# Performance work log

Measured on AMD Instinct MI355X. Metric: run time of the kernel, lower is better.

Reference implementation:

```python
import jax, jax.numpy as jnp
import numpy as np

N, E = 50000, 800000
HID, EDGE_DIM, HEADS = 128, 16, 4
C = HID // HEADS  # 32
NEG_SLOPE = 0.2  # GATv2Conv default negative_slope


def setup_inputs() -> dict:
    key = jax.random.key(0)
    ks = jax.random.split(key, 16)
    def glorot(k, shape):
        fan_in = shape[0]
        return jax.random.normal(k, shape, jnp.float32) / np.sqrt(fan_in)
    return {
        "x": jax.random.normal(ks[0], (N, HID), jnp.float32),
        "edge_index": jax.random.randint(ks[1], (2, E), 0, N, jnp.int64 if jax.config.jax_enable_x64 else jnp.int32),
        "edge_attr": jax.random.normal(ks[2], (E, EDGE_DIM), jnp.float32),
        # GATv2Conv params (lin_l, lin_r with bias; lin_edge bias-free; att; final bias)
        "Wl": glorot(ks[3], (HID, HID)),
        "bl": jnp.zeros((HID,), jnp.float32),
        "Wr": glorot(ks[4], (HID, HID)),
        "br": jnp.zeros((HID,), jnp.float32),
        "We": glorot(ks[5], (EDGE_DIM, HID)),
        "att": glorot(ks[6], (HEADS, C)),
        "bias_gat": jnp.zeros((HID,), jnp.float32),
        # RMSNorm weights
        "w_norm1": jnp.ones((HID,), jnp.float32),
        "w_norm2": jnp.ones((HID,), jnp.float32),
        # FFN params
        "ffn_w1": glorot(ks[7], (HID, 4 * HID)),
        "ffn_b1": jnp.zeros((4 * HID,), jnp.float32),
        "ffn_w2": glorot(ks[8], (4 * HID, HID)),
        "ffn_b2": jnp.zeros((HID,), jnp.float32),
    }


def rmsnorm(x, w):
    # torch.nn.RMSNorm with eps=None -> eps = finfo(dtype).eps
    eps = jnp.finfo(x.dtype).eps
    ms = jnp.mean(x * x, axis=-1, keepdims=True)
    return x * jax.lax.rsqrt(ms + eps) * w


def gatv2_conv(x, edge_index, edge_attr, Wl, bl, Wr, br, We, att, bias_gat):
    n = x.shape[0]
    h, c = att.shape
    xl = (x @ Wl + bl).reshape(n, h, c)   # source-side transform (x_j)
    xr = (x @ Wr + br).reshape(n, h, c)   # target-side transform (x_i)
    src, dst = edge_index[0], edge_index[1]
    e = (edge_attr @ We).reshape(-1, h, c)
    m = xl[src] + xr[dst] + e                       # [E, H, C] per-edge message pre-activation
    s = jnp.where(m > 0, m, NEG_SLOPE * m)          # LeakyReLU(0.2)
    logits = jnp.einsum('ehc,hc->eh', s, att)       # [E, H]
    # scatter-softmax over edges grouped by target node
    lmax = jax.ops.segment_max(logits, dst, num_segments=n)
    ex = jnp.exp(logits - lmax[dst])
    den = jax.ops.segment_sum(ex, dst, num_segments=n)
    alpha = ex / (den[dst] + 1e-16)                 # PyG softmax denominator guard
    out = jax.ops.segment_sum(alpha[..., None] * xl[src], dst, num_segments=n)
    return out.reshape(n, h * c) + bias_gat


def reference(x, edge_index, edge_attr, Wl, bl, Wr, br, We, att, bias_gat,
              w_norm1, w_norm2, ffn_w1, ffn_b1, ffn_w2, ffn_b2):
    x_attn = gatv2_conv(x, edge_index, edge_attr, Wl, bl, Wr, br, We, att, bias_gat)
    h = rmsnorm(x + x_attn, w_norm1)
    f = jax.nn.gelu(h @ ffn_w1 + ffn_b1, approximate=False) @ ffn_w2 + ffn_b2
    return rmsnorm(h + f, w_norm2)
```

## Files before the change

kernel.cpp:

```cpp
#include <hip/hip_runtime.h>

#define NN 50000
#define EE 800000

typedef unsigned short u16;

#define OFF_GAT  0u
#define OFF_XLB  6400000u
#define OFF_XRB  9600000u
#define OFF_SRC  12800000u
#define OFF_EID  13600000u
#define OFF_CNT  14400000u
#define OFF_OFS  14450000u
#define OFF_H    6400000u
#define OFF_WLRT 14500004u
#define OFF_W1T  14516388u
#define OFF_W2T  14549156u

#define RMS_EPS 1.1920928955078125e-7f

typedef float f32x4v __attribute__((ext_vector_type(4)));
typedef short s16x8 __attribute__((ext_vector_type(8)));

__device__ __forceinline__ f32x4v mfma16(s16x8 a, s16x8 b, f32x4v c) {
  return __builtin_amdgcn_mfma_f32_16x16x32_bf16(a, b, c, 0, 0, 0);
}
__device__ __forceinline__ u16 f2b(float f) {
  unsigned int u = __float_as_uint(f);
  unsigned int r = (u + 0x7fffu + ((u >> 16) & 1u)) >> 16;
  return (u16)r;
}
__device__ __forceinline__ float b2f(u16 u) {
  union { float f; unsigned int i; } x; x.i = ((unsigned int)u) << 16; return x.f;
}
__device__ __forceinline__ s16x8 ld_bf16x8_f32(const float* __restrict__ p) {
  float4 v0 = *(const float4*)p;
  float4 v1 = *(const float4*)(p + 4);
  s16x8 r;
  r[0] = (short)f2b(v0.x); r[1] = (short)f2b(v0.y);
  r[2] = (short)f2b(v0.z); r[3] = (short)f2b(v0.w);
  r[4] = (short)f2b(v1.x); r[5] = (short)f2b(v1.y);
  r[6] = (short)f2b(v1.z); r[7] = (short)f2b(v1.w);
  return r;
}
__device__ __forceinline__ float readlane_f32(float v, int lane) {
  return __int_as_float(__builtin_amdgcn_readlane(__float_as_int(v), lane));
}
__device__ __forceinline__ int readlane_i32(int v, int lane) {
  return __builtin_amdgcn_readlane(v, lane);
}

__global__ __launch_bounds__(256) void k_zero(int* __restrict__ p, int n) {
  int i = blockIdx.x * 256 + threadIdx.x;
  if (i < n) p[i] = 0;
}
__global__ __launch_bounds__(256) void k_tcvt2(const float* __restrict__ Wl, const float* __restrict__ Wr,
                                               u16* __restrict__ out) {
  int i = blockIdx.x * 256 + threadIdx.x;
  int n = i >> 7, k = i & 127;
  float v = (n < 128) ? Wl[k * 128 + n] : Wr[k * 128 + (n - 128)];
  out[i] = f2b(v);
}
__global__ __launch_bounds__(256) void k_t1(const float* __restrict__ W1, u16* __restrict__ out) {
  int i = blockIdx.x * 256 + threadIdx.x;
  int n = i >> 7, k = i & 127;
  out[i] = f2b(W1[k * 512 + n]);
}
__global__ __launch_bounds__(256) void k_t2(const float* __restrict__ W2, u16* __restrict__ out) {
  int i = blockIdx.x * 256 + threadIdx.x;
  int n = i >> 9, k = i & 511;
  out[i] = f2b(W2[k * 128 + n]);
}

__global__ __launch_bounds__(256) void k_hist(const int* __restrict__ ei, int* __restrict__ cnt) {
  int e = blockIdx.x * 256 + threadIdx.x;
  if (e < EE) atomicAdd(&cnt[ei[EE + e]], 1);
}

__global__ __launch_bounds__(1024) void k_scan(const int* __restrict__ cnt,
    int* __restrict__ offs, int* __restrict__ pos)
{
  __shared__ int wsum[16];
  __shared__ int carry_s;
  int tid = threadIdx.x, lane = tid & 63, wv = tid >> 6;
  if (tid == 0) carry_s = 0;
  __syncthreads();
  for (int base = 0; base < NN; base += 1024) {
    int i = base + tid;
    int v = (i < NN) ? cnt[i] : 0;
    int x = v;
#pragma unroll
    for (int ofs = 1; ofs < 64; ofs <<= 1) {
      int y = __shfl_up(x, ofs);
      if (lane >= ofs) x += y;
    }
    if (lane == 63) wsum[wv] = x;
    __syncthreads();
    if (wv == 0) {
      int s = (lane < 16) ? wsum[lane] : 0;
#pragma unroll
      for (int ofs = 1; ofs < 16; ofs <<= 1) {
        int y = __shfl_up(s, ofs);
        if (lane >= ofs) s += y;
      }
      if (lane < 16) wsum[lane] = s;
    }
    __syncthreads();
    int wbase = (wv > 0) ? wsum[wv - 1] : 0;
    int incl = x + wbase + carry_s;
    if (i < NN) { offs[i + 1] = incl; pos[i] = incl - v; }
    if (base == 0 && tid == 0) offs[0] = 0;
    __syncthreads();
    if (tid == 1023) carry_s = incl;
    __syncthreads();
  }
}

__global__ __launch_bounds__(256) void k_permute(const int* __restrict__ ei,
    int* __restrict__ pos, int* __restrict__ srcarr, int* __restrict__ eidarr)
{
  int e = blockIdx.x * 256 + threadIdx.x;
  if (e < EE) {
    int slot = atomicAdd(&pos[ei[EE + e]], 1);
    srcarr[slot] = ei[e];
    eidarr[slot] = e;
  }
}

__global__ __launch_bounds__(256) void k1_mfma(const float* __restrict__ x, const u16* __restrict__ wlrt,
    const float* __restrict__ bl, const float* __restrict__ br,
    u16* __restrict__ xlb, u16* __restrict__ xrb)
{
  int tid = threadIdx.x;
  int w = tid >> 6, lane = tid & 63;
  int quad = lane >> 4, l16 = lane & 15;
  int row0 = blockIdx.x * 32;
  int ko = quad * 8;
  f32x4v acc[2][4];
#pragma unroll
  for (int mt = 0; mt < 2; ++mt)
#pragma unroll
    for (int nt = 0; nt < 4; ++nt) acc[mt][nt] = (f32x4v){0.f, 0.f, 0.f, 0.f};
#pragma unroll
  for (int ks = 0; ks < 4; ++ks) {
    int k0 = ks * 32 + ko;
    s16x8 a[2];
#pragma unroll
    for (int mt = 0; mt < 2; ++mt) {
      int row = row0 + mt * 16 + l16; if (row >= NN) row = NN - 1;
      a[mt] = ld_bf16x8_f32(x + row * 128 + k0);
    }
#pragma unroll
    for (int nt = 0; nt < 4; ++nt) {
      int col = w * 64 + nt * 16 + l16;
      s16x8 b = *(const s16x8*)(wlrt + col * 128 + k0);
      acc[0][nt] = mfma16(a[0], b, acc[0][nt]);
      acc[1][nt] = mfma16(a[1], b, acc[1][nt]);
    }
  }
#pragma unroll
  for (int nt = 0; nt < 4; ++nt) {
    int col = w * 64 + nt * 16 + l16;
    bool isl = col < 128;
    float bias = isl ? bl[col] : br[col - 128];
    u16* dst = isl ? xlb : xrb;
    int cc = isl ? col : col - 128;
#pragma unroll
    for (int mt = 0; mt < 2; ++mt)
#pragma unroll
      for (int r = 0; r < 4; ++r) {
        int row = row0 + mt * 16 + quad * 4 + r;
        if (row < NN) dst[row * 128 + cc] = f2b(acc[mt][nt][r] + bias);
      }
  }
}

__global__ __launch_bounds__(256) void k2_attn(
    const int* __restrict__ offs, const int* __restrict__ srcarr,
    const int* __restrict__ eidarr, const float* __restrict__ eattr,
    const float* __restrict__ att, const float* __restrict__ We,
    const u16* __restrict__ xlb, const u16* __restrict__ xrb,
    float* __restrict__ gat)
{
  int l = threadIdx.x & 63;
  int wid = (blockIdx.x * blockDim.x + threadIdx.x) >> 6;
  int nw = (gridDim.x * blockDim.x) >> 6;
  int c0 = 2 * l;
  const float2* We2 = (const float2*)We;
  float2 wef[16];
#pragma unroll
  for (int k = 0; k < 16; ++k) wef[k] = We2[k * 64 + l];
  float a0 = att[c0], a1 = att[c0 + 1];
  for (int d = wid; d < NN; d += nw) {
    int start = offs[d];
    int deg = offs[d + 1] - start;
    ushort2 xru = *(const ushort2*)(xrb + d * 128 + c0);
    float xr0 = b2f(xru.x), xr1 = b2f(xru.y);
    float mh = -1e30f, lh = 0.f, O0 = 0.f, O1 = 0.f;
    for (int base = 0; base < deg; base += 64) {
      bool act = (base + l) < deg;
      int idx = start + base + l;
      int sv = act ? srcarr[idx] : 0;
      int ev = act ? eidarr[idx] : 0;
      int cnt = min(64, deg - base);
      for (int sub = 0; sub < cnt; sub += 4) {
        int eidq = __shfl(ev, sub + (l >> 4));
        float eav = eattr[eidq * 16 + (l & 15)];
#pragma unroll
        for (int j2 = 0; j2 < 4; ++j2) {
          int j = sub + j2;
          if (j >= cnt) break;
          int sr = readlane_i32(sv, j);
          float ep0 = 0.f, ep1 = 0.f;
#pragma unroll
          for (int k = 0; k < 16; ++k) {
            float ek = readlane_f32(eav, j2 * 16 + k);
            ep0 = fmaf(ek, wef[k].x, ep0);
            ep1 = fmaf(ek, wef[k].y, ep1);
          }
          ushort2 xlu = *(const ushort2*)(xlb + sr * 128 + c0);
          float xl0 = b2f(xlu.x), xl1 = b2f(xlu.y);
          float m0 = xl0 + xr0 + ep0;
          float m1 = xl1 + xr1 + ep1;
          float s0 = m0 > 0.f ? m0 : 0.2f * m0;
          float s1 = m1 > 0.f ? m1 : 0.2f * m1;
          float p = fmaf(s0, a0, s1 * a1);
          p += __shfl_xor(p, 1); p += __shfl_xor(p, 2);
          p += __shfl_xor(p, 4); p += __shfl_xor(p, 8);
          float nm = fmaxf(mh, p);
          float sc = __expf(mh - nm);
          float wgt = __expf(p - nm);
          lh = lh * sc + wgt;
          O0 = fmaf(wgt, xl0, O0 * sc);
          O1 = fmaf(wgt, xl1, O1 * sc);
          mh = nm;
        }
      }
    }
    float inv = 1.f / (lh + 1e-16f);
    *(float2*)(gat + d * 128 + c0) = make_float2(O0 * inv, O1 * inv);
  }
}

__global__ __launch_bounds__(256) void k5_norm1(const float* __restrict__ x,
    const float* __restrict__ gat, const float* __restrict__ bg,
    const float* __restrict__ wn1, float* __restrict__ h)
{
  int l = threadIdx.x & 63;
  int row = blockIdx.x * 4 + (threadIdx.x >> 6);
  int c0 = 2 * l;
  float2 xu = *(const float2*)(x + row * 128 + c0);
  float2 gv = *(const float2*)(gat + row * 128 + c0);
  float2 bu = *(const float2*)(bg + c0);
  float v0 = xu.x + gv.x + bu.x;
  float v1 = xu.y + gv.y + bu.y;
  float ss = v0 * v0 + v1 * v1;
#pragma unroll
  for (int o = 1; o < 64; o <<= 1) ss += __shfl_xor(ss, o);
  float rr = rsqrtf(ss * (1.f / 128.f) + RMS_EPS);
  float2 wu = *(const float2*)(wn1 + c0);
  *(float2*)(h + row * 128 + c0) = make_float2(v0 * rr * wu.x, v1 * rr * wu.y);
}

__global__ __launch_bounds__(256) void k6_mfma(const float* __restrict__ h,
    const u16* __restrict__ w1t, const u16* __restrict__ w2t,
    const float* __restrict__ b1, const float* __restrict__ b2,
    const float* __restrict__ wn2, float* __restrict__ out)
{
  __shared__ u16 tls[32 * 520];
  __shared__ float red[4][32];
  int tid = threadIdx.x;
  int w = tid >> 6, lane = tid & 63;
  int quad = lane >> 4, l16 = lane & 15;
  int row0 = blockIdx.x * 32;
  int ko = quad * 8;

  f32x4v acc1[2][8];
#pragma unroll
  for (int mt = 0; mt < 2; ++mt)
#pragma unroll
    for (int nt = 0; nt < 8; ++nt) acc1[mt][nt] = (f32x4v){0.f, 0.f, 0.f, 0.f};
#pragma unroll
  for (int ks = 0; ks < 4; ++ks) {
    int k0 = ks * 32 + ko;
    s16x8 a[2];
#pragma unroll
    for (int mt = 0; mt < 2; ++mt) {
      int row = row0 + mt * 16 + l16; if (row >= NN) row = NN - 1;
      a[mt] = ld_bf16x8_f32(h + row * 128 + k0);
    }
#pragma unroll
    for (int nt = 0; nt < 8; ++nt) {
      int col = w * 128 + nt * 16 + l16;
      s16x8 b = *(const s16x8*)(w1t + col * 128 + k0);
      acc1[0][nt] = mfma16(a[0], b, acc1[0][nt]);
      acc1[1][nt] = mfma16(a[1], b, acc1[1][nt]);
    }
  }
#pragma unroll
  for (int nt = 0; nt < 8; ++nt) {
    int col = w * 128 + nt * 16 + l16;
    float bb = b1[col];
#pragma unroll
    for (int mt = 0; mt < 2; ++mt)
#pragma unroll
      for (int r = 0; r < 4; ++r) {
        float t = acc1[mt][nt][r] + bb;
        t = 0.5f * t * (1.f + erff(t * 0.70710678118654752f));
        tls[(mt * 16 + quad * 4 + r) * 520 + col] = f2b(t);
      }
  }
  __syncthreads();

  f32x4v acc2[2][2];
#pragma unroll
  for (int mt = 0; mt < 2; ++mt)
#pragma unroll
    for (int nt = 0; nt < 2; ++nt) acc2[mt][nt] = (f32x4v){0.f, 0.f, 0.f, 0.f};
#pragma unroll
  for (int ks = 0; ks < 16; ++ks) {
    int k0 = ks * 32 + ko;
    s16x8 a2[2];
#pragma unroll
    for (int mt = 0; mt < 2; ++mt)
      a2[mt] = *(const s16x8*)(tls + (mt * 16 + l16) * 520 + k0);
#pragma unroll
    for (int nt = 0; nt < 2; ++nt) {
      int col = w * 32 + nt * 16 + l16;
      s16x8 b = *(const s16x8*)(w2t + col * 512 + k0);
      acc2[0][nt] = mfma16(a2[0], b, acc2[0][nt]);
      acc2[1][nt] = mfma16(a2[1], b, acc2[1][nt]);
    }
  }
  int cols[2]; float bb2[2], wn[2];
#pragma unroll
  for (int nt = 0; nt < 2; ++nt) {
    cols[nt] = w * 32 + nt * 16 + l16;
    bb2[nt] = b2[cols[nt]];
    wn[nt] = wn2[cols[nt]];
  }
  float ov[2][2][4];
#pragma unroll
  for (int mt = 0; mt < 2; ++mt)
#pragma unroll
    for (int r = 0; r < 4; ++r) {
      int row = row0 + mt * 16 + quad * 4 + r;
      int rowc = row < NN ? row : NN - 1;
#pragma unroll
      for (int nt = 0; nt < 2; ++nt)
        ov[mt][nt][r] = h[rowc * 128 + cols[nt]] + acc2[mt][nt][r] + bb2[nt];
    }
#pragma unroll
  for (int mt = 0; mt < 2; ++mt)
#pragma unroll
    for (int r = 0; r < 4; ++r) {
      float q = ov[mt][0][r] * ov[mt][0][r] + ov[mt][1][r] * ov[mt][1][r];
      q += __shfl_xor(q, 1); q += __shfl_xor(q, 2);
      q += __shfl_xor(q, 4); q += __shfl_xor(q, 8);
      if (l16 == 0) red[w][mt * 16 + quad * 4 + r] = q;
    }
  __syncthreads();
#pragma unroll
  for (int mt = 0; mt < 2; ++mt)
#pragma unroll
    for (int r = 0; r < 4; ++r) {
      int rl = mt * 16 + quad * 4 + r;
      float tot = red[0][rl] + red[1][rl] + red[2][rl] + red[3][rl];
      float rr = rsqrtf(tot * (1.f / 128.f) + RMS_EPS);
      int row = row0 + rl;
      if (row < NN) {
        out[row * 128 + cols[0]] = ov[mt][0][r] * rr * wn[0];
        out[row * 128 + cols[1]] = ov[mt][1][r] * rr * wn[1];
      }
    }
}

extern "C" void kernel_launch(void* const* d_in, const int* in_sizes, int n_in,
                              void* d_out, int out_size, void* d_ws, size_t ws_size,
                              hipStream_t stream) {
  const float* x   = (const float*)d_in[0];
  const int*   ei  = (const int*)d_in[1];
  const float* ea  = (const float*)d_in[2];
  const float* Wl  = (const float*)d_in[3];
  const float* bl  = (const float*)d_in[4];
  const float* Wr  = (const float*)d_in[5];
  const float* br  = (const float*)d_in[6];
  const float* We  = (const float*)d_in[7];
  const float* att = (const float*)d_in[8];
  const float* bg  = (const float*)d_in[9];
  const float* wn1 = (const float*)d_in[10];
  const float* wn2 = (const float*)d_in[11];
  const float* W1  = (const float*)d_in[12];
  const float* b1  = (const float*)d_in[13];
  const float* W2  = (const float*)d_in[14];
  const float* b2  = (const float*)d_in[15];

  float* wsf = (float*)d_ws;
  int*   wsi = (int*)d_ws;

  float* gat  = wsf + OFF_GAT;
  u16* xlb    = (u16*)(wsf + OFF_XLB);
  u16* xrb    = (u16*)(wsf + OFF_XRB);
  int* srcarr = wsi + OFF_SRC;
  int* eidarr = wsi + OFF_EID;
  int* cnt    = wsi + OFF_CNT;
  int* pos    = wsi + OFF_CNT;
  int* offs   = wsi + OFF_OFS;
  float* hbuf = wsf + OFF_H;
  u16* wlrt   = (u16*)(wsf + OFF_WLRT);
  u16* w1t    = (u16*)(wsf + OFF_W1T);
  u16* w2t    = (u16*)(wsf + OFF_W2T);

  k_zero<<<(NN + 255) / 256, 256, 0, stream>>>(cnt, NN);
  k_tcvt2<<<128, 256, 0, stream>>>(Wl, Wr, wlrt);
  k_t1<<<256, 256, 0, stream>>>(W1, w1t);
  k_t2<<<256, 256, 0, stream>>>(W2, w2t);

  k_hist<<<(EE + 255) / 256, 256, 0, stream>>>(ei, cnt);
  k_scan<<<1, 1024, 0, stream>>>(cnt, offs, pos);
  k_permute<<<(EE + 255) / 256, 256, 0, stream>>>(ei, pos, srcarr, eidarr);

  k1_mfma<<<(NN + 31) / 32, 256, 0, stream>>>(x, wlrt, bl, br, xlb, xrb);

  k2_attn<<<1024, 256, 0, stream>>>(offs, srcarr, eidarr, ea, att, We, xlb, xrb, gat);

  k5_norm1<<<NN / 4, 256, 0, stream>>>(x, gat, bg, wn1, hbuf);

  k6_mfma<<<(NN + 31) / 32, 256, 0, stream>>>(hbuf, w1t, w2t, b1, b2, wn2, (float*)d_out);
}
```

Before: 586.9 us.

## Batch online-softmax updates per four edges, pack src/eid, fuse prep kernels

```diff
diff --git a/kernel.cpp b/kernel.cpp
--- a/kernel.cpp
+++ b/kernel.cpp
@@ -8,8 +8,7 @@
 #define OFF_GAT  0u
 #define OFF_XLB  6400000u
 #define OFF_XRB  9600000u
-#define OFF_SRC  12800000u
-#define OFF_EID  13600000u
+#define OFF_SE   12800000u
 #define OFF_CNT  14400000u
 #define OFF_OFS  14450000u
 #define OFF_H    6400000u
@@ -50,26 +49,25 @@
   return __builtin_amdgcn_readlane(v, lane);
 }
 
-__global__ __launch_bounds__(256) void k_zero(int* __restrict__ p, int n) {
+__global__ __launch_bounds__(256) void k_prep(const float* __restrict__ Wl, const float* __restrict__ Wr,
+    const float* __restrict__ W1, const float* __restrict__ W2,
+    int* __restrict__ cnt, u16* __restrict__ wlrt, u16* __restrict__ w1t, u16* __restrict__ w2t)
+{
   int i = blockIdx.x * 256 + threadIdx.x;
-  if (i < n) p[i] = 0;
-}
-__global__ __launch_bounds__(256) void k_tcvt2(const float* __restrict__ Wl, const float* __restrict__ Wr,
-                                               u16* __restrict__ out) {
-  int i = blockIdx.x * 256 + threadIdx.x;
-  int n = i >> 7, k = i & 127;
-  float v = (n < 128) ? Wl[k * 128 + n] : Wr[k * 128 + (n - 128)];
-  out[i] = f2b(v);
-}
-__global__ __launch_bounds__(256) void k_t1(const float* __restrict__ W1, u16* __restrict__ out) {
-  int i = blockIdx.x * 256 + threadIdx.x;
-  int n = i >> 7, k = i & 127;
-  out[i] = f2b(W1[k * 512 + n]);
-}
-__global__ __launch_bounds__(256) void k_t2(const float* __restrict__ W2, u16* __restrict__ out) {
-  int i = blockIdx.x * 256 + threadIdx.x;
-  int n = i >> 9, k = i & 511;
-  out[i] = f2b(W2[k * 128 + n]);
+  if (i < NN) cnt[i] = 0;
+  if (i < 32768) {
+    int n = i >> 7, k = i & 127;
+    float v = (n < 128) ? Wl[k * 128 + n] : Wr[k * 128 + (n - 128)];
+    wlrt[i] = f2b(v);
+  }
+  {
+    int n = i >> 7, k = i & 127;
+    w1t[i] = f2b(W1[k * 512 + n]);
+  }
+  {
+    int n = i >> 9, k = i & 511;
+    w2t[i] = f2b(W2[k * 128 + n]);
+  }
 }
 
 __global__ __launch_bounds__(256) void k_hist(const int* __restrict__ ei, int* __restrict__ cnt) {
@@ -117,13 +115,12 @@
 }
 
 __global__ __launch_bounds__(256) void k_permute(const int* __restrict__ ei,
-    int* __restrict__ pos, int* __restrict__ srcarr, int* __restrict__ eidarr)
+    int* __restrict__ pos, int2* __restrict__ se)
 {
   int e = blockIdx.x * 256 + threadIdx.x;
   if (e < EE) {
     int slot = atomicAdd(&pos[ei[EE + e]], 1);
-    srcarr[slot] = ei[e];
-    eidarr[slot] = e;
+    se[slot] = make_int2(ei[e], e);
   }
 }
 
@@ -176,8 +173,8 @@
 }
 
 __global__ __launch_bounds__(256) void k2_attn(
-    const int* __restrict__ offs, const int* __restrict__ srcarr,
-    const int* __restrict__ eidarr, const float* __restrict__ eattr,
+    const int* __restrict__ offs, const int2* __restrict__ se,
+    const float* __restrict__ eattr,
     const float* __restrict__ att, const float* __restrict__ We,
     const u16* __restrict__ xlb, const u16* __restrict__ xrb,
     float* __restrict__ gat)
@@ -200,17 +197,14 @@
     for (int base = 0; base < deg; base += 64) {
       bool act = (base + l) < deg;
       int idx = start + base + l;
-      int sv = act ? srcarr[idx] : 0;
-      int ev = act ? eidarr[idx] : 0;
+      int2 sev = act ? se[idx] : make_int2(0, 0);
       int cnt = min(64, deg - base);
       for (int sub = 0; sub < cnt; sub += 4) {
-        int eidq = __shfl(ev, sub + (l >> 4));
+        int eidq = __shfl(sev.y, sub + (l >> 4));
         float eav = eattr[eidq * 16 + (l & 15)];
+        float p[4], xl0v[4], xl1v[4];
 #pragma unroll
         for (int j2 = 0; j2 < 4; ++j2) {
-          int j = sub + j2;
-          if (j >= cnt) break;
-          int sr = readlane_i32(sv, j);
           float ep0 = 0.f, ep1 = 0.f;
 #pragma unroll
           for (int k = 0; k < 16; ++k) {
@@ -218,23 +212,33 @@
             ep0 = fmaf(ek, wef[k].x, ep0);
             ep1 = fmaf(ek, wef[k].y, ep1);
           }
+          int sr = readlane_i32(sev.x, sub + j2);
           ushort2 xlu = *(const ushort2*)(xlb + sr * 128 + c0);
           float xl0 = b2f(xlu.x), xl1 = b2f(xlu.y);
           float m0 = xl0 + xr0 + ep0;
           float m1 = xl1 + xr1 + ep1;
           float s0 = m0 > 0.f ? m0 : 0.2f * m0;
           float s1 = m1 > 0.f ? m1 : 0.2f * m1;
-          float p = fmaf(s0, a0, s1 * a1);
-          p += __shfl_xor(p, 1); p += __shfl_xor(p, 2);
-          p += __shfl_xor(p, 4); p += __shfl_xor(p, 8);
-          float nm = fmaxf(mh, p);
-          float sc = __expf(mh - nm);
-          float wgt = __expf(p - nm);
-          lh = lh * sc + wgt;
-          O0 = fmaf(wgt, xl0, O0 * sc);
-          O1 = fmaf(wgt, xl1, O1 * sc);
-          mh = nm;
+          p[j2] = fmaf(s0, a0, s1 * a1);
+          xl0v[j2] = xl0; xl1v[j2] = xl1;
         }
+#pragma unroll
+        for (int o = 1; o <= 8; o <<= 1) {
+          p[0] += __shfl_xor(p[0], o);
+          p[1] += __shfl_xor(p[1], o);
+          p[2] += __shfl_xor(p[2], o);
+          p[3] += __shfl_xor(p[3], o);
+        }
+#pragma unroll
+        for (int j2 = 0; j2 < 4; ++j2) if (sub + j2 >= cnt) p[j2] = -1e30f;
+        float nm = fmaxf(fmaxf(fmaxf(p[0], p[1]), fmaxf(p[2], p[3])), mh);
+        float sc = __expf(mh - nm);
+        float w0 = __expf(p[0] - nm), w1 = __expf(p[1] - nm);
+        float w2 = __expf(p[2] - nm), w3 = __expf(p[3] - nm);
+        lh = fmaf(lh, sc, (w0 + w1) + (w2 + w3));
+        O0 = fmaf(O0, sc, fmaf(w0, xl0v[0], fmaf(w1, xl0v[1], fmaf(w2, xl0v[2], w3 * xl0v[3]))));
+        O1 = fmaf(O1, sc, fmaf(w0, xl1v[0], fmaf(w1, xl1v[1], fmaf(w2, xl1v[2], w3 * xl1v[3]))));
+        mh = nm;
       }
     }
     float inv = 1.f / (lh + 1e-16f);
@@ -401,8 +405,7 @@
   float* gat  = wsf + OFF_GAT;
   u16* xlb    = (u16*)(wsf + OFF_XLB);
   u16* xrb    = (u16*)(wsf + OFF_XRB);
-  int* srcarr = wsi + OFF_SRC;
-  int* eidarr = wsi + OFF_EID;
+  int2* se    = (int2*)(wsf + OFF_SE);
   int* cnt    = wsi + OFF_CNT;
   int* pos    = wsi + OFF_CNT;
   int* offs   = wsi + OFF_OFS;
@@ -411,18 +414,15 @@
   u16* w1t    = (u16*)(wsf + OFF_W1T);
   u16* w2t    = (u16*)(wsf + OFF_W2T);
 
-  k_zero<<<(NN + 255) / 256, 256, 0, stream>>>(cnt, NN);
-  k_tcvt2<<<128, 256, 0, stream>>>(Wl, Wr, wlrt);
-  k_t1<<<256, 256, 0, stream>>>(W1, w1t);
-  k_t2<<<256, 256, 0, stream>>>(W2, w2t);
+  k_prep<<<256, 256, 0, stream>>>(Wl, Wr, W1, W2, cnt, wlrt, w1t, w2t);
 
   k_hist<<<(EE + 255) / 256, 256, 0, stream>>>(ei, cnt);
   k_scan<<<1, 1024, 0, stream>>>(cnt, offs, pos);
-  k_permute<<<(EE + 255) / 256, 256, 0, stream>>>(ei, pos, srcarr, eidarr);
+  k_permute<<<(EE + 255) / 256, 256, 0, stream>>>(ei, pos, se);
 
   k1_mfma<<<(NN + 31) / 32, 256, 0, stream>>>(x, wlrt, bl, br, xlb, xrb);
 
-  k2_attn<<<1024, 256, 0, stream>>>(offs, srcarr, eidarr, ea, att, We, xlb, xrb, gat);
+  k2_attn<<<2048, 256, 0, stream>>>(offs, se, ea, att, We, xlb, xrb, gat);
 
   k5_norm1<<<NN / 4, 256, 0, stream>>>(x, gat, bg, wn1, hbuf);
 
```

Result: faster. 550.5 us (-6.2%).
